# Kernel optimization log

Measured on AMD Instinct MI355X. Metric: run time of the kernel, lower is better.

Reference implementation:

```python
import jax, jax.numpy as jnp
import numpy as np


def _hungarian_cols(cost):
    """Jonker-Volgenant / Hungarian (same optimum as scipy.linear_sum_assignment).
    cost: [n, n] numpy. Returns cols[i] = column assigned to row i."""
    cost = np.asarray(cost, dtype=np.float64)
    n = cost.shape[0]
    INF = np.inf
    u = np.zeros(n + 1)
    v = np.zeros(n + 1)
    p = np.zeros(n + 1, dtype=np.int64)   # p[j]: row matched to column j (1-based; 0=free)
    way = np.zeros(n + 1, dtype=np.int64)
    for i in range(1, n + 1):
        p[0] = i
        j0 = 0
        minv = np.full(n + 1, INF)
        used = np.zeros(n + 1, dtype=bool)
        while True:
            used[j0] = True
            i0 = p[j0]
            cand = cost[i0 - 1] - u[i0] - v[1:]
            free = ~used[1:]
            upd = free & (cand < minv[1:])
            minv[1:][upd] = cand[upd]
            way[1:][upd] = j0
            masked = np.where(free, minv[1:], INF)
            j1 = int(np.argmin(masked)) + 1
            delta = masked[j1 - 1]
            u[p[used]] += delta
            v[used] -= delta
            minv[~used] -= delta
            j0 = j1
            if p[j0] == 0:
                break
        while j0:
            j1 = way[j0]
            p[j0] = p[j1]
            j0 = j1
    cols = np.empty(n, dtype=np.int64)
    cols[p[1:] - 1] = np.arange(n)
    return cols


def _cdist(x, y):
    # batched euclidean distance (p=2), [B,N,D] x [B,M,D] -> [B,N,M]
    x2 = jnp.sum(x * x, axis=-1)[:, :, None]
    y2 = jnp.sum(y * y, axis=-1)[:, None, :]
    d2 = x2 + y2 - 2.0 * jnp.einsum('bnd,bmd->bnm', x, y)
    return jnp.sqrt(jnp.maximum(d2, 0.0))


def setup_inputs() -> dict:
    key = jax.random.key(0)
    k1, k2, k3 = jax.random.split(key, 3)
    B, N, D = 64, 128, 2048
    return {
        'inputs': jax.random.normal(k1, (B, N, D), dtype=jnp.float32),
        'stacked_outputs': jax.random.normal(k2, (B, N, D), dtype=jnp.float32),
        'member_probabilities': jax.random.uniform(k3, (B, N, 1), dtype=jnp.float32),
    }


def reference(inputs, stacked_outputs, member_probabilities):
    # cost matrices computed with no grad in the original (detached)
    cost = np.asarray(jax.device_get(_cdist(inputs, stacked_outputs)))
    cols = jnp.asarray(np.stack([_hungarian_cols(c) for c in cost]))  # [B, N]
    # output_mapping (match_matrix[...,None]*outputs[None,...]).sum(1) == gather rows by cols
    mapped_outputs = jnp.take_along_axis(stacked_outputs, cols[:, :, None], axis=1)
    mapped_prob = jnp.take_along_axis(member_probabilities, cols[:, :, None], axis=1)
    return mapped_outputs, mapped_prob, cols
```

## Files before the change

### kernel.cpp

```cpp
#include <hip/hip_runtime.h>

#define NB 64
#define NN 128
#define ND 2048

__global__ __launch_bounds__(256) void cost_kernel(const float* __restrict__ X,
                                                   const float* __restrict__ Y,
                                                   float* __restrict__ cost) {
  const int b  = blockIdx.x >> 2;
  const int rt = blockIdx.x & 3;
  const int rbase = rt * 32;
  __shared__ float Xs[32][33];
  __shared__ float Ys[32][129];
  __shared__ float xsq_s[32];
  __shared__ float ysq_s[128];
  const int tid = threadIdx.x;
  const int tr = tid >> 5;
  const int tc = tid & 31;
  float acc[4][4] = {{0.f,0.f,0.f,0.f},{0.f,0.f,0.f,0.f},
                     {0.f,0.f,0.f,0.f},{0.f,0.f,0.f,0.f}};
  float xsq[4] = {0.f,0.f,0.f,0.f};
  float ysq[4] = {0.f,0.f,0.f,0.f};
  const float* Xb = X + ((size_t)(b * NN + rbase)) * ND;
  const float* Yb = Y + ((size_t)(b * NN)) * ND;
  const int lrow = tid >> 3;
  const int lkk  = (tid & 7) << 2;

  for (int kb = 0; kb < ND; kb += 32) {
    __syncthreads();
    {
      float4 xv = *(const float4*)(Xb + (size_t)lrow * ND + kb + lkk);
      Xs[lkk + 0][lrow] = xv.x; Xs[lkk + 1][lrow] = xv.y;
      Xs[lkk + 2][lrow] = xv.z; Xs[lkk + 3][lrow] = xv.w;
    }
#pragma unroll
    for (int l = 0; l < 4; ++l) {
      int idx = tid + 256 * l;
      int col = idx >> 3;
      int kk  = (idx & 7) << 2;
      float4 yv = *(const float4*)(Yb + (size_t)col * ND + kb + kk);
      Ys[kk + 0][col] = yv.x; Ys[kk + 1][col] = yv.y;
      Ys[kk + 2][col] = yv.z; Ys[kk + 3][col] = yv.w;
    }
    __syncthreads();
#pragma unroll 4
    for (int kk = 0; kk < 32; ++kk) {
      float xv[4], yv[4];
#pragma unroll
      for (int ii = 0; ii < 4; ++ii) xv[ii] = Xs[kk][4 * tr + ii];
#pragma unroll
      for (int jj = 0; jj < 4; ++jj) yv[jj] = Ys[kk][tc + 32 * jj];
#pragma unroll
      for (int ii = 0; ii < 4; ++ii) xsq[ii] += xv[ii] * xv[ii];
#pragma unroll
      for (int jj = 0; jj < 4; ++jj) ysq[jj] += yv[jj] * yv[jj];
#pragma unroll
      for (int ii = 0; ii < 4; ++ii)
#pragma unroll
        for (int jj = 0; jj < 4; ++jj)
          acc[ii][jj] += xv[ii] * yv[jj];
    }
  }
  if (tc == 0) {
#pragma unroll
    for (int ii = 0; ii < 4; ++ii) xsq_s[4 * tr + ii] = xsq[ii];
  }
  if (tr == 0) {
#pragma unroll
    for (int jj = 0; jj < 4; ++jj) ysq_s[tc + 32 * jj] = ysq[jj];
  }
  __syncthreads();
#pragma unroll
  for (int ii = 0; ii < 4; ++ii) {
    int r = rbase + 4 * tr + ii;
    float xs = xsq_s[4 * tr + ii];
#pragma unroll
    for (int jj = 0; jj < 4; ++jj) {
      int c = tc + 32 * jj;
      float d2 = xs + ysq_s[c] - 2.0f * acc[ii][jj];
      cost[((size_t)(b * NN + r)) * NN + c] = sqrtf(fmaxf(d2, 0.0f));
    }
  }
}

__device__ __forceinline__ unsigned umin2(unsigned a, unsigned b) { return a < b ? a : b; }
__device__ __forceinline__ unsigned umax2(unsigned a, unsigned b) { return a > b ? a : b; }

__device__ __forceinline__ unsigned wave_min_u32(unsigned x) {
  unsigned t;
  t = (unsigned)__builtin_amdgcn_update_dpp((int)x, (int)x, 0x111, 0xF, 0xF, false); x = umin2(x, t);
  t = (unsigned)__builtin_amdgcn_update_dpp((int)x, (int)x, 0x112, 0xF, 0xF, false); x = umin2(x, t);
  t = (unsigned)__builtin_amdgcn_update_dpp((int)x, (int)x, 0x114, 0xF, 0xF, false); x = umin2(x, t);
  t = (unsigned)__builtin_amdgcn_update_dpp((int)x, (int)x, 0x118, 0xF, 0xF, false); x = umin2(x, t);
  t = (unsigned)__builtin_amdgcn_update_dpp((int)x, (int)x, 0x142, 0xA, 0xF, false); x = umin2(x, t);
  t = (unsigned)__builtin_amdgcn_update_dpp((int)x, (int)x, 0x143, 0xC, 0xF, false); x = umin2(x, t);
  return (unsigned)__builtin_amdgcn_readlane((int)x, 63);
}

template <int CTRL, int RMASK>
__device__ __forceinline__ void min2_step(unsigned& a, unsigned& b) {
  unsigned ap = (unsigned)__builtin_amdgcn_update_dpp((int)a, (int)a, CTRL, RMASK, 0xF, false);
  unsigned bp = (unsigned)__builtin_amdgcn_update_dpp((int)b, (int)b, CTRL, RMASK, 0xF, false);
  unsigned hi = umax2(a, ap);
  a = umin2(a, ap);
  b = umin2(umin2(b, bp), hi);
}

__device__ __forceinline__ void wave_min2_u32(unsigned a, unsigned b,
                                              unsigned& m1k, unsigned& m2k) {
  min2_step<0x111, 0xF>(a, b);
  min2_step<0x112, 0xF>(a, b);
  min2_step<0x114, 0xF>(a, b);
  min2_step<0x118, 0xF>(a, b);
  min2_step<0x142, 0xA>(a, b);
  min2_step<0x143, 0xC>(a, b);
  m1k = (unsigned)__builtin_amdgcn_readlane((int)a, 63);
  m2k = (unsigned)__builtin_amdgcn_readlane((int)b, 63);
}

__device__ __forceinline__ double readlane_f64(double d, int lane) {
  int lo = __builtin_amdgcn_readlane(__double2loint(d), lane);
  int hi = __builtin_amdgcn_readlane(__double2hiint(d), lane);
  return __hiloint2double(hi, lo);
}

__global__ __launch_bounds__(64) void hungarian_kernel(const float* __restrict__ cost,
                                                       int* __restrict__ cols) {
  const int b = blockIdx.x;
  const int lane = threadIdx.x;
  __shared__ float cst[NN * NN];
  __shared__ int colrow[NN];
  __shared__ int rwin[NN];
  __shared__ double u_row[NN + 1];
  __shared__ int queue[4 * NN + 8];
  __shared__ int qcnt[1];

  {
    const float4* src = (const float4*)(cost + (size_t)b * NN * NN);
    float4* dst = (float4*)cst;
    for (int t = lane; t < NN * NN / 4; t += 64) dst[t] = src[t];
  }
  for (int t = lane; t <= NN; t += 64) u_row[t] = 0.0;
  __syncthreads();

  float cmin[2]; int cargr[2];
#pragma unroll
  for (int k2 = 0; k2 < 2; ++k2) {
    const int j = lane + 64 * k2;
    float mn = cst[j]; int ar = 0;
    for (int r = 1; r < NN; ++r) {
      float cr = cst[r * NN + j];
      if (cr < mn) { mn = cr; ar = r; }
    }
    cmin[k2] = mn; cargr[k2] = ar;
    colrow[j] = ar;
  }
  __syncthreads();
  int rowwin[2] = {-1, -1};
  for (int j = 0; j < NN; ++j) {
    int rr = colrow[j];
#pragma unroll
    for (int k2 = 0; k2 < 2; ++k2) {
      if (rr == lane + 64 * k2 && rowwin[k2] < 0) rowwin[k2] = j;
    }
  }
#pragma unroll
  for (int k2 = 0; k2 < 2; ++k2) rwin[lane + 64 * k2] = rowwin[k2];
  const unsigned long long mask0 = __ballot(rowwin[0] >= 0);
  const unsigned long long mask1 = __ballot(rowwin[1] >= 0);
  __syncthreads();

  int    p_[2];
  double pu_[2], v_[2];
#pragma unroll
  for (int k2 = 0; k2 < 2; ++k2) {
    const int j = lane + 64 * k2;
    const int r = cargr[k2];
    p_[k2]  = (rwin[r] == j) ? (r + 1) : 0;
    pu_[k2] = 0.0;
    v_[k2]  = (double)cmin[k2];
  }

  for (int i = 1; i <= NN; ++i) {
    const bool matched = (i - 1) < 64 ? ((mask0 >> (i - 1)) & 1ull)
                                      : ((mask1 >> (i - 65)) & 1ull);
    if (!matched) continue;
    const int j1 = rwin[i - 1];
    const float* crow = &cst[(i - 1) * NN];
    double d0 = (double)crow[lane]      - v_[0];
    double d1 = (double)crow[lane + 64] - v_[1];
    if (lane == (j1 & 63)) { if (j1 >> 6) d1 = 1e300; else d0 = 1e300; }
    const double dmn = fmin(d0, d1);
    const unsigned k = __float_as_uint((float)dmn);
    const unsigned mk = wave_min_u32(k);
    const unsigned long long bm = __ballot(k == mk);
    const int wl = (int)__ffsll(bm) - 1;
    const double mu = readlane_f64(dmn, wl);
    if (lane == (j1 & 63)) {
      if (j1 >> 6) { v_[1] -= mu; pu_[1] = mu; }
      else         { v_[0] -= mu; pu_[0] = mu; }
    }
  }

  if (lane == 0) {
    int t = 0;
    for (int r = 1; r <= NN; ++r) {
      const bool m = (r - 1) < 64 ? ((mask0 >> (r - 1)) & 1ull)
                                  : ((mask1 >> (r - 65)) & 1ull);
      if (!m) queue[t++] = r;
    }
    qcnt[0] = t;
  }
  __syncthreads();
  {
    int head = 0, tail = qcnt[0];
    for (int pops = 0; head < tail && pops < 3 * NN; ++pops) {
      const int i = queue[head++];
      const float* crow = cst + (i - 1) * NN;
      const double d0 = (double)crow[lane]      - v_[0];
      const double d1 = (double)crow[lane + 64] - v_[1];
      double dmn, dmx; int jmn;
      if (d1 < d0) { dmn = d1; dmx = d0; jmn = lane + 64; }
      else         { dmn = d0; dmx = d1; jmn = lane; }
      const unsigned ka = __float_as_uint((float)dmn);
      const unsigned kb = __float_as_uint((float)dmx);
      unsigned m1k, m2k;
      wave_min2_u32(ka, kb, m1k, m2k);
      const unsigned long long bA = __ballot(ka == m1k);
      const int win = (int)__ffsll(bA) - 1;
      const double m1 = readlane_f64(dmn, win);
      const int j1 = __builtin_amdgcn_readlane(jmn, win);
      const unsigned long long bA2 = __ballot(ka == m2k) & ~(1ull << win);
      const unsigned long long bB2 = __ballot(kb == m2k);
      const int lA = bA2 ? (int)__ffsll(bA2) - 1 : 64;
      const int lB = bB2 ? (int)__ffsll(bB2) - 1 : 64;
      double m2 = (lA <= lB) ? readlane_f64(dmn, lA < 64 ? lA : 63)
                             : readlane_f64(dmx, lB < 64 ? lB : 63);
      m2 = fmax(m2, m1);
      const int own = j1 & 63, hk = j1 >> 6;
      const int    psel  = hk ? p_[1]  : p_[0];
      const double pusel = hk ? pu_[1] : pu_[0];
      const int kk = __builtin_amdgcn_readlane(psel, own);
      const double oldpu = readlane_f64(pusel, own);
      if (lane == own) {
        if (hk) { v_[1] -= (m2 - m1); p_[1] = i; pu_[1] = m2; }
        else    { v_[0] -= (m2 - m1); p_[0] = i; pu_[0] = m2; }
      }
      if (lane == 0) {
        u_row[i] = m2;
        if (kk != 0) { u_row[kk] = oldpu; queue[tail] = kk; }
      }
      if (kk != 0) ++tail;
      __syncthreads();
    }
  }
  __syncthreads();

  for (int t = lane; t < NN; t += 64) colrow[t] = 0;
  __syncthreads();
  if (p_[0] > 0) colrow[p_[0] - 1] = 1;
  if (p_[1] > 0) colrow[p_[1] - 1] = 1;
  __syncthreads();
  const unsigned long long fmask0 = __ballot(colrow[lane] == 0);
  const unsigned long long fmask1 = __ballot(colrow[lane + 64] == 0);

  const unsigned INFBITS = 0x7f800000u;

  for (int i = 1; i <= NN; ++i) {
    const bool freerow = (i - 1) < 64 ? ((fmask0 >> (i - 1)) & 1ull)
                                      : ((fmask1 >> (i - 65)) & 1ull);
    if (!freerow) continue;

    const double u_i = u_row[i];
    double D_[2]; int way_[2]; int used_[2] = {0, 0};
    {
      const float* crow = &cst[(i - 1) * NN];
      D_[0] = (double)crow[lane]      - u_i - v_[0];  way_[0] = 0;
      D_[1] = (double)crow[lane + 64] - u_i - v_[1];  way_[1] = 0;
    }
    double Dfinal = 0.0; int jF = 1;
    for (int it = 0; it < NN + 2; ++it) {
      const float pr0 = used_[0] ? __uint_as_float(INFBITS) : fmaxf((float)D_[0], 0.0f);
      const float pr1 = used_[1] ? __uint_as_float(INFBITS) : fmaxf((float)D_[1], 0.0f);
      const int   k2l = (pr1 < pr0) ? 1 : 0;
      const unsigned key = __float_as_uint(k2l ? pr1 : pr0);
      const unsigned rmin = wave_min_u32(key);
      const unsigned long long wm = __ballot(key == rmin);
      const int winlane = (int)__ffsll(wm) - 1;
      const int metal = ((k2l ? p_[1] : p_[0]) << 1) | k2l;
      const int meta = __builtin_amdgcn_readlane(metal, winlane);
      const int i0 = meta >> 1;
      const int k2w = meta & 1;
      const int bj = 1 + winlane + (k2w << 6);
      const float* crow = &cst[((i0 - 1) & 127) * NN];
      const float c0 = crow[lane];
      const float c1 = crow[lane + 64];
      const double bv = readlane_f64(k2l ? D_[1] : D_[0], winlane);
      if (i0 == 0) { Dfinal = bv; jF = bj; break; }
      const double u0 = readlane_f64(k2l ? pu_[1] : pu_[0], winlane);
      if (lane == winlane) { if (k2w) used_[1] = 1; else used_[0] = 1; }
      const double base = bv - u0;
      if (!used_[0]) {
        const double cand = (double)c0 + base - v_[0];
        if (cand < D_[0]) { D_[0] = cand; way_[0] = bj; }
      }
      if (!used_[1]) {
        const double cand = (double)c1 + base - v_[1];
        if (cand < D_[1]) { D_[1] = cand; way_[1] = bj; }
      }
    }
#pragma unroll
    for (int k2 = 0; k2 < 2; ++k2) {
      if (used_[k2]) {
        const double diff = Dfinal - D_[k2];
        v_[k2]  -= diff;
        pu_[k2] += diff;
      }
    }
    int j = jF;
    for (int g = 0; g < NN + 2; ++g) {
      const int own = (j - 1) & 63;
      const int hk  = (j - 1) >> 6;
      const int wsel = hk ? way_[1] : way_[0];
      const int wj = __builtin_amdgcn_readlane(wsel, own);
      int pn; double pun;
      if (wj == 0) { pn = i; pun = u_i + Dfinal; }
      else {
        const int o2 = (wj - 1) & 63, h2 = (wj - 1) >> 6;
        const int    psel2  = h2 ? p_[1]  : p_[0];
        const double pusel2 = h2 ? pu_[1] : pu_[0];
        pn  = __builtin_amdgcn_readlane(psel2, o2);
        pun = readlane_f64(pusel2, o2);
      }
      if (lane == own) {
        if (hk) { p_[1] = pn; pu_[1] = pun; }
        else    { p_[0] = pn; pu_[0] = pun; }
      }
      if (wj == 0) break;
      j = wj;
    }
  }

#pragma unroll
  for (int k2 = 0; k2 < 2; ++k2) {
    const int r = p_[k2] - 1;
    if (r >= 0 && r < NN) cols[b * NN + r] = lane + 64 * k2;
  }
}

__global__ __launch_bounds__(256) void gather_kernel(const float* __restrict__ outs,
                                                     const float* __restrict__ probs,
                                                     const int* __restrict__ cols,
                                                     float* __restrict__ out) {
  const int bi = blockIdx.x;
  const int b  = bi >> 7;
  const int col = cols[bi] & (NN - 1);
  const float4* src = (const float4*)(outs + ((size_t)(b * NN + col)) * ND);
  float4* dst = (float4*)(out + (size_t)bi * ND);
  const int t = threadIdx.x;
  dst[t]       = src[t];
  dst[t + 256] = src[t + 256];
  if (t == 0) {
    const size_t PROB_OFF = (size_t)NB * NN * ND;
    out[PROB_OFF + bi]        = probs[b * NN + col];
    out[PROB_OFF + 8192 + bi] = (float)(cols[bi] & (NN - 1));
  }
}

extern "C" void kernel_launch(void* const* d_in, const int* in_sizes, int n_in,
                              void* d_out, int out_size, void* d_ws, size_t ws_size,
                              hipStream_t stream) {
  const float* X = (const float*)d_in[0];
  const float* Y = (const float*)d_in[1];
  const float* P = (const float*)d_in[2];
  float* out = (float*)d_out;

  float* cost = (float*)d_ws;
  int* cols = (int*)((char*)d_ws + (size_t)NB * NN * NN * 4);

  cost_kernel<<<dim3(NB * 4), dim3(256), 0, stream>>>(X, Y, cost);
  hungarian_kernel<<<dim3(NB), dim3(64), 0, stream>>>(cost, cols);
  gather_kernel<<<dim3(NB * NN), dim3(256), 0, stream>>>(Y, P, cols, out);
}
```

Baseline: 696.1 us.

## Split cost tiles finer and prefetch rows in Hungarian auction and augment loops

The cost kernel now uses 16-row tiles, which doubles the grid to 512 blocks so more of the GPU's compute units have work. The cost is that the Y tile is reloaded twice as often. In the Hungarian kernel's auction phase, the next queued row's costs are prefetched into registers and the per-pop __syncthreads is dropped, since the block is a single wave. In the shortest-path loop, the base value is computed before the reduction and read with a single readlane, and the early-exit check moves ahead of the cost-row load to shorten the serial dependency chain.

Result: slower. 717.0 us (+3.0%).

```diff
diff --git a/kernel.cpp b/kernel.cpp
--- a/kernel.cpp
+++ b/kernel.cpp
@@ -7,19 +7,18 @@
 __global__ __launch_bounds__(256) void cost_kernel(const float* __restrict__ X,
                                                    const float* __restrict__ Y,
                                                    float* __restrict__ cost) {
-  const int b  = blockIdx.x >> 2;
-  const int rt = blockIdx.x & 3;
-  const int rbase = rt * 32;
-  __shared__ float Xs[32][33];
+  const int b  = blockIdx.x >> 3;
+  const int rt = blockIdx.x & 7;
+  const int rbase = rt * 16;
+  __shared__ float Xs[32][17];
   __shared__ float Ys[32][129];
-  __shared__ float xsq_s[32];
+  __shared__ float xsq_s[16];
   __shared__ float ysq_s[128];
   const int tid = threadIdx.x;
   const int tr = tid >> 5;
   const int tc = tid & 31;
-  float acc[4][4] = {{0.f,0.f,0.f,0.f},{0.f,0.f,0.f,0.f},
-                     {0.f,0.f,0.f,0.f},{0.f,0.f,0.f,0.f}};
-  float xsq[4] = {0.f,0.f,0.f,0.f};
+  float acc[2][4] = {{0.f,0.f,0.f,0.f},{0.f,0.f,0.f,0.f}};
+  float xsq[2] = {0.f,0.f};
   float ysq[4] = {0.f,0.f,0.f,0.f};
   const float* Xb = X + ((size_t)(b * NN + rbase)) * ND;
   const float* Yb = Y + ((size_t)(b * NN)) * ND;
@@ -28,7 +27,7 @@
 
   for (int kb = 0; kb < ND; kb += 32) {
     __syncthreads();
-    {
+    if (tid < 128) {
       float4 xv = *(const float4*)(Xb + (size_t)lrow * ND + kb + lkk);
       Xs[lkk + 0][lrow] = xv.x; Xs[lkk + 1][lrow] = xv.y;
       Xs[lkk + 2][lrow] = xv.z; Xs[lkk + 3][lrow] = xv.w;
@@ -45,17 +44,17 @@
     __syncthreads();
 #pragma unroll 4
     for (int kk = 0; kk < 32; ++kk) {
-      float xv[4], yv[4];
-#pragma unroll
-      for (int ii = 0; ii < 4; ++ii) xv[ii] = Xs[kk][4 * tr + ii];
+      float xv[2], yv[4];
+#pragma unroll
+      for (int ii = 0; ii < 2; ++ii) xv[ii] = Xs[kk][2 * tr + ii];
 #pragma unroll
       for (int jj = 0; jj < 4; ++jj) yv[jj] = Ys[kk][tc + 32 * jj];
 #pragma unroll
-      for (int ii = 0; ii < 4; ++ii) xsq[ii] += xv[ii] * xv[ii];
+      for (int ii = 0; ii < 2; ++ii) xsq[ii] += xv[ii] * xv[ii];
 #pragma unroll
       for (int jj = 0; jj < 4; ++jj) ysq[jj] += yv[jj] * yv[jj];
 #pragma unroll
-      for (int ii = 0; ii < 4; ++ii)
+      for (int ii = 0; ii < 2; ++ii)
 #pragma unroll
         for (int jj = 0; jj < 4; ++jj)
           acc[ii][jj] += xv[ii] * yv[jj];
@@ -63,7 +62,7 @@
   }
   if (tc == 0) {
 #pragma unroll
-    for (int ii = 0; ii < 4; ++ii) xsq_s[4 * tr + ii] = xsq[ii];
+    for (int ii = 0; ii < 2; ++ii) xsq_s[2 * tr + ii] = xsq[ii];
   }
   if (tr == 0) {
 #pragma unroll
@@ -71,9 +70,9 @@
   }
   __syncthreads();
 #pragma unroll
-  for (int ii = 0; ii < 4; ++ii) {
-    int r = rbase + 4 * tr + ii;
-    float xs = xsq_s[4 * tr + ii];
+  for (int ii = 0; ii < 2; ++ii) {
+    int r = rbase + 2 * tr + ii;
+    float xs = xsq_s[2 * tr + ii];
 #pragma unroll
     for (int jj = 0; jj < 4; ++jj) {
       int c = tc + 32 * jj;
@@ -214,11 +213,18 @@
   __syncthreads();
   {
     int head = 0, tail = qcnt[0];
+    int i_cur = 0; float c0_cur = 0.f, c1_cur = 0.f;
+    if (head < tail) {
+      i_cur  = queue[head];
+      c0_cur = cst[(i_cur - 1) * NN + lane];
+      c1_cur = cst[(i_cur - 1) * NN + lane + 64];
+    }
     for (int pops = 0; head < tail && pops < 3 * NN; ++pops) {
-      const int i = queue[head++];
-      const float* crow = cst + (i - 1) * NN;
-      const double d0 = (double)crow[lane]      - v_[0];
-      const double d1 = (double)crow[lane + 64] - v_[1];
+      const int i = i_cur;
+      ++head;
+      int i_nxt = (head < tail) ? queue[head] : -1;
+      const double d0 = (double)c0_cur - v_[0];
+      const double d1 = (double)c1_cur - v_[1];
       double dmn, dmx; int jmn;
       if (d1 < d0) { dmn = d1; dmx = d0; jmn = lane + 64; }
       else         { dmn = d0; dmx = d1; jmn = lane; }
@@ -251,7 +257,12 @@
         if (kk != 0) { u_row[kk] = oldpu; queue[tail] = kk; }
       }
       if (kk != 0) ++tail;
-      __syncthreads();
+      if (i_nxt < 0) i_nxt = kk;
+      if (head < tail) {
+        c0_cur = cst[(i_nxt - 1) * NN + lane];
+        c1_cur = cst[(i_nxt - 1) * NN + lane + 64];
+        i_cur = i_nxt;
+      }
     }
   }
   __syncthreads();
@@ -284,6 +295,8 @@
       const float pr1 = used_[1] ? __uint_as_float(INFBITS) : fmaxf((float)D_[1], 0.0f);
       const int   k2l = (pr1 < pr0) ? 1 : 0;
       const unsigned key = __float_as_uint(k2l ? pr1 : pr0);
+      const double Dsel  = k2l ? D_[1]  : D_[0];
+      const double basec = Dsel - (k2l ? pu_[1] : pu_[0]);
       const unsigned rmin = wave_min_u32(key);
       const unsigned long long wm = __ballot(key == rmin);
       const int winlane = (int)__ffsll(wm) - 1;
@@ -292,14 +305,12 @@
       const int i0 = meta >> 1;
       const int k2w = meta & 1;
       const int bj = 1 + winlane + (k2w << 6);
-      const float* crow = &cst[((i0 - 1) & 127) * NN];
+      if (i0 == 0) { Dfinal = readlane_f64(Dsel, winlane); jF = bj; break; }
+      const float* crow = &cst[(i0 - 1) * NN];
       const float c0 = crow[lane];
       const float c1 = crow[lane + 64];
-      const double bv = readlane_f64(k2l ? D_[1] : D_[0], winlane);
-      if (i0 == 0) { Dfinal = bv; jF = bj; break; }
-      const double u0 = readlane_f64(k2l ? pu_[1] : pu_[0], winlane);
+      const double base = readlane_f64(basec, winlane);
       if (lane == winlane) { if (k2w) used_[1] = 1; else used_[0] = 1; }
-      const double base = bv - u0;
       if (!used_[0]) {
         const double cand = (double)c0 + base - v_[0];
         if (cand < D_[0]) { D_[0] = cand; way_[0] = bj; }
@@ -378,7 +389,7 @@
   float* cost = (float*)d_ws;
   int* cols = (int*)((char*)d_ws + (size_t)NB * NN * NN * 4);
 
-  cost_kernel<<<dim3(NB * 4), dim3(256), 0, stream>>>(X, Y, cost);
+  cost_kernel<<<dim3(NB * 8), dim3(256), 0, stream>>>(X, Y, cost);
   hungarian_kernel<<<dim3(NB), dim3(64), 0, stream>>>(cost, cols);
   gather_kernel<<<dim3(NB * NN), dim3(256), 0, stream>>>(Y, P, cols, out);
 }
```

## Retile cost kernel to 64x64 block tiles with 8x2 per-thread accumulators

Applied to the files above, without the earlier changes.

Each block of the distance kernel now computes a 64x64 tile of the cost matrix instead of 32 rows by 128 columns. Each thread holds an 8x2 accumulator and reads X with float4 loads from shared memory. This balances the X and Y load volume per block, cuts global Y traffic per block, and lowers LDS read instructions per FMA. In exchange the shared-memory layout changes, and the X tile rows are padded to 72 floats to keep the float4 reads aligned.

After: 706.9 us. About the same (+1.6%).

```diff
diff --git a/kernel.cpp b/kernel.cpp
--- a/kernel.cpp
+++ b/kernel.cpp
@@ -8,76 +8,78 @@
                                                    const float* __restrict__ Y,
                                                    float* __restrict__ cost) {
   const int b  = blockIdx.x >> 2;
-  const int rt = blockIdx.x & 3;
-  const int rbase = rt * 32;
-  __shared__ float Xs[32][33];
-  __shared__ float Ys[32][129];
-  __shared__ float xsq_s[32];
-  __shared__ float ysq_s[128];
+  const int rt = (blockIdx.x >> 1) & 1;
+  const int ct = blockIdx.x & 1;
+  const int rbase = rt * 64;
+  const int cbase = ct * 64;
+  __shared__ float Xs[32][72];
+  __shared__ float Ys[32][65];
+  __shared__ float xsq_s[64];
+  __shared__ float ysq_s[64];
   const int tid = threadIdx.x;
   const int tr = tid >> 5;
   const int tc = tid & 31;
-  float acc[4][4] = {{0.f,0.f,0.f,0.f},{0.f,0.f,0.f,0.f},
-                     {0.f,0.f,0.f,0.f},{0.f,0.f,0.f,0.f}};
-  float xsq[4] = {0.f,0.f,0.f,0.f};
-  float ysq[4] = {0.f,0.f,0.f,0.f};
+  float acc[8][2] = {};
+  float xsq[8] = {};
+  float ysq[2] = {};
   const float* Xb = X + ((size_t)(b * NN + rbase)) * ND;
-  const float* Yb = Y + ((size_t)(b * NN)) * ND;
-  const int lrow = tid >> 3;
-  const int lkk  = (tid & 7) << 2;
+  const float* Yb = Y + ((size_t)(b * NN + cbase)) * ND;
 
   for (int kb = 0; kb < ND; kb += 32) {
     __syncthreads();
-    {
-      float4 xv = *(const float4*)(Xb + (size_t)lrow * ND + kb + lkk);
-      Xs[lkk + 0][lrow] = xv.x; Xs[lkk + 1][lrow] = xv.y;
-      Xs[lkk + 2][lrow] = xv.z; Xs[lkk + 3][lrow] = xv.w;
-    }
-#pragma unroll
-    for (int l = 0; l < 4; ++l) {
-      int idx = tid + 256 * l;
-      int col = idx >> 3;
-      int kk  = (idx & 7) << 2;
-      float4 yv = *(const float4*)(Yb + (size_t)col * ND + kb + kk);
-      Ys[kk + 0][col] = yv.x; Ys[kk + 1][col] = yv.y;
-      Ys[kk + 2][col] = yv.z; Ys[kk + 3][col] = yv.w;
+#pragma unroll
+    for (int l = 0; l < 2; ++l) {
+      const int idx = tid + 256 * l;
+      const int row = idx >> 3;
+      const int kk4 = (idx & 7) << 2;
+      float4 v = *(const float4*)(Xb + (size_t)row * ND + kb + kk4);
+      Xs[kk4 + 0][row] = v.x; Xs[kk4 + 1][row] = v.y;
+      Xs[kk4 + 2][row] = v.z; Xs[kk4 + 3][row] = v.w;
+    }
+#pragma unroll
+    for (int l = 0; l < 2; ++l) {
+      const int idx = tid + 256 * l;
+      const int col = idx >> 3;
+      const int kk4 = (idx & 7) << 2;
+      float4 v = *(const float4*)(Yb + (size_t)col * ND + kb + kk4);
+      Ys[kk4 + 0][col] = v.x; Ys[kk4 + 1][col] = v.y;
+      Ys[kk4 + 2][col] = v.z; Ys[kk4 + 3][col] = v.w;
     }
     __syncthreads();
 #pragma unroll 4
     for (int kk = 0; kk < 32; ++kk) {
-      float xv[4], yv[4];
-#pragma unroll
-      for (int ii = 0; ii < 4; ++ii) xv[ii] = Xs[kk][4 * tr + ii];
-#pragma unroll
-      for (int jj = 0; jj < 4; ++jj) yv[jj] = Ys[kk][tc + 32 * jj];
-#pragma unroll
-      for (int ii = 0; ii < 4; ++ii) xsq[ii] += xv[ii] * xv[ii];
-#pragma unroll
-      for (int jj = 0; jj < 4; ++jj) ysq[jj] += yv[jj] * yv[jj];
-#pragma unroll
-      for (int ii = 0; ii < 4; ++ii)
-#pragma unroll
-        for (int jj = 0; jj < 4; ++jj)
+      const float4 xa = *(const float4*)&Xs[kk][8 * tr];
+      const float4 xb = *(const float4*)&Xs[kk][8 * tr + 4];
+      const float xv[8] = {xa.x, xa.y, xa.z, xa.w, xb.x, xb.y, xb.z, xb.w};
+      const float yv[2] = {Ys[kk][tc], Ys[kk][tc + 32]};
+#pragma unroll
+      for (int ii = 0; ii < 8; ++ii) xsq[ii] += xv[ii] * xv[ii];
+#pragma unroll
+      for (int jj = 0; jj < 2; ++jj) ysq[jj] += yv[jj] * yv[jj];
+#pragma unroll
+      for (int ii = 0; ii < 8; ++ii)
+#pragma unroll
+        for (int jj = 0; jj < 2; ++jj)
           acc[ii][jj] += xv[ii] * yv[jj];
     }
   }
   if (tc == 0) {
 #pragma unroll
-    for (int ii = 0; ii < 4; ++ii) xsq_s[4 * tr + ii] = xsq[ii];
+    for (int ii = 0; ii < 8; ++ii) xsq_s[8 * tr + ii] = xsq[ii];
   }
   if (tr == 0) {
 #pragma unroll
-    for (int jj = 0; jj < 4; ++jj) ysq_s[tc + 32 * jj] = ysq[jj];
-  }
-  __syncthreads();
-#pragma unroll
-  for (int ii = 0; ii < 4; ++ii) {
-    int r = rbase + 4 * tr + ii;
-    float xs = xsq_s[4 * tr + ii];
-#pragma unroll
-    for (int jj = 0; jj < 4; ++jj) {
-      int c = tc + 32 * jj;
-      float d2 = xs + ysq_s[c] - 2.0f * acc[ii][jj];
+    for (int jj = 0; jj < 2; ++jj) ysq_s[tc + 32 * jj] = ysq[jj];
+  }
+  __syncthreads();
+#pragma unroll
+  for (int ii = 0; ii < 8; ++ii) {
+    const int r = rbase + 8 * tr + ii;
+    const float xs = xsq_s[8 * tr + ii];
+#pragma unroll
+    for (int jj = 0; jj < 2; ++jj) {
+      const int c = cbase + tc + 32 * jj;
+      const float d2 = xs + ysq_s[tc + 32 * jj] - 2.0f * acc[ii][jj];
       cost[((size_t)(b * NN + r)) * NN + c] = sqrtf(fmaxf(d2, 0.0f));
     }
   }
```

## Hold Hungarian cost matrix in VGPRs with switch-based row lookup instead of LDS

Applied to the files above, without the earlier changes.

Each lane now keeps its two cost columns (256 floats) in registers instead of staging the whole 128x128 matrix in shared memory. Every row access in the Hungarian phases becomes a 128-way switch on the row index that selects the register pair. The aim is to drop the 64KB of LDS traffic and its latency from the serial augmenting loop. The cost is very high register pressure with possible spills, plus a jump-table branch on every row access in place of a single LDS load.

New measurement: 930.9 us. +33.7%, slower.

```diff
diff --git a/kernel.cpp b/kernel.cpp
--- a/kernel.cpp
+++ b/kernel.cpp
@@ -124,36 +124,57 @@
   return __hiloint2double(hi, lo);
 }
 
-__global__ __launch_bounds__(64) void hungarian_kernel(const float* __restrict__ cost,
-                                                       int* __restrict__ cols) {
+#define RL_CASE(R) case R: rlC0 = creg[2*(R)]; rlC1 = creg[2*(R)+1]; break;
+#define RL_C4(B)  RL_CASE(B) RL_CASE((B)+1) RL_CASE((B)+2) RL_CASE((B)+3)
+#define RL_C16(B) RL_C4(B) RL_C4((B)+4) RL_C4((B)+8) RL_C4((B)+12)
+#define RL_C64(B) RL_C16(B) RL_C16((B)+16) RL_C16((B)+32) RL_C16((B)+48)
+#define ROW_LOOKUP(RIDX, OUT0, OUT1)                               \
+  do {                                                             \
+    float rlC0 = 0.f, rlC1 = 0.f;                                  \
+    switch (RIDX) {                                                \
+      RL_C64(0) RL_C64(64)                                         \
+      default: break;                                              \
+    }                                                              \
+    OUT0 = rlC0; OUT1 = rlC1;                                      \
+  } while (0)
+
+__global__ __launch_bounds__(64, 1) void hungarian_kernel(const float* __restrict__ cost,
+                                                          int* __restrict__ cols) {
   const int b = blockIdx.x;
   const int lane = threadIdx.x;
-  __shared__ float cst[NN * NN];
   __shared__ int colrow[NN];
   __shared__ int rwin[NN];
   __shared__ double u_row[NN + 1];
   __shared__ int queue[4 * NN + 8];
   __shared__ int qcnt[1];
 
+  float creg[2 * NN];
   {
-    const float4* src = (const float4*)(cost + (size_t)b * NN * NN);
-    float4* dst = (float4*)cst;
-    for (int t = lane; t < NN * NN / 4; t += 64) dst[t] = src[t];
-  }
+    const float* src = cost + (size_t)b * NN * NN;
+#pragma unroll
+    for (int r = 0; r < NN; ++r) {
+      creg[2 * r]     = src[r * NN + lane];
+      creg[2 * r + 1] = src[r * NN + lane + 64];
+    }
+  }
+#pragma unroll
+  for (int t = 0; t < 2 * NN; ++t) asm volatile("" : "+v"(creg[t]));
+
   for (int t = lane; t <= NN; t += 64) u_row[t] = 0.0;
   __syncthreads();
 
   float cmin[2]; int cargr[2];
-#pragma unroll
-  for (int k2 = 0; k2 < 2; ++k2) {
-    const int j = lane + 64 * k2;
-    float mn = cst[j]; int ar = 0;
+  {
+    float mn0 = creg[0], mn1 = creg[1];
+    int a0 = 0, a1 = 0;
+#pragma unroll
     for (int r = 1; r < NN; ++r) {
-      float cr = cst[r * NN + j];
-      if (cr < mn) { mn = cr; ar = r; }
-    }
-    cmin[k2] = mn; cargr[k2] = ar;
-    colrow[j] = ar;
+      const float c0 = creg[2 * r], c1 = creg[2 * r + 1];
+      if (c0 < mn0) { mn0 = c0; a0 = r; }
+      if (c1 < mn1) { mn1 = c1; a1 = r; }
+    }
+    cmin[0] = mn0; cmin[1] = mn1; cargr[0] = a0; cargr[1] = a1;
+    colrow[lane] = a0; colrow[lane + 64] = a1;
   }
   __syncthreads();
   int rowwin[2] = {-1, -1};
@@ -186,9 +207,10 @@
                                       : ((mask1 >> (i - 65)) & 1ull);
     if (!matched) continue;
     const int j1 = rwin[i - 1];
-    const float* crow = &cst[(i - 1) * NN];
-    double d0 = (double)crow[lane]      - v_[0];
-    double d1 = (double)crow[lane + 64] - v_[1];
+    float c0r, c1r;
+    ROW_LOOKUP(i - 1, c0r, c1r);
+    double d0 = (double)c0r - v_[0];
+    double d1 = (double)c1r - v_[1];
     if (lane == (j1 & 63)) { if (j1 >> 6) d1 = 1e300; else d0 = 1e300; }
     const double dmn = fmin(d0, d1);
     const unsigned k = __float_as_uint((float)dmn);
@@ -216,9 +238,10 @@
     int head = 0, tail = qcnt[0];
     for (int pops = 0; head < tail && pops < 3 * NN; ++pops) {
       const int i = queue[head++];
-      const float* crow = cst + (i - 1) * NN;
-      const double d0 = (double)crow[lane]      - v_[0];
-      const double d1 = (double)crow[lane + 64] - v_[1];
+      float c0r, c1r;
+      ROW_LOOKUP(i - 1, c0r, c1r);
+      const double d0 = (double)c0r - v_[0];
+      const double d1 = (double)c1r - v_[1];
       double dmn, dmx; int jmn;
       if (d1 < d0) { dmn = d1; dmx = d0; jmn = lane + 64; }
       else         { dmn = d0; dmx = d1; jmn = lane; }
@@ -274,9 +297,10 @@
     const double u_i = u_row[i];
     double D_[2]; int way_[2]; int used_[2] = {0, 0};
     {
-      const float* crow = &cst[(i - 1) * NN];
-      D_[0] = (double)crow[lane]      - u_i - v_[0];  way_[0] = 0;
-      D_[1] = (double)crow[lane + 64] - u_i - v_[1];  way_[1] = 0;
+      float c0r, c1r;
+      ROW_LOOKUP(i - 1, c0r, c1r);
+      D_[0] = (double)c0r - u_i - v_[0];  way_[0] = 0;
+      D_[1] = (double)c1r - u_i - v_[1];  way_[1] = 0;
     }
     double Dfinal = 0.0; int jF = 1;
     for (int it = 0; it < NN + 2; ++it) {
@@ -292,20 +316,19 @@
       const int i0 = meta >> 1;
       const int k2w = meta & 1;
       const int bj = 1 + winlane + (k2w << 6);
-      const float* crow = &cst[((i0 - 1) & 127) * NN];
-      const float c0 = crow[lane];
-      const float c1 = crow[lane + 64];
       const double bv = readlane_f64(k2l ? D_[1] : D_[0], winlane);
       if (i0 == 0) { Dfinal = bv; jF = bj; break; }
+      float c0r, c1r;
+      ROW_LOOKUP((i0 - 1) & 127, c0r, c1r);
       const double u0 = readlane_f64(k2l ? pu_[1] : pu_[0], winlane);
       if (lane == winlane) { if (k2w) used_[1] = 1; else used_[0] = 1; }
       const double base = bv - u0;
       if (!used_[0]) {
-        const double cand = (double)c0 + base - v_[0];
+        const double cand = (double)c0r + base - v_[0];
         if (cand < D_[0]) { D_[0] = cand; way_[0] = bj; }
       }
       if (!used_[1]) {
-        const double cand = (double)c1 + base - v_[1];
+        const double cand = (double)c1r + base - v_[1];
         if (cand < D_[1]) { D_[1] = cand; way_[1] = bj; }
       }
     }
```
